# Kernel optimization log

Measured on AMD Instinct MI355X. Metric: run time of the kernel, lower is better.

## Reference

```python
import jax, jax.numpy as jnp
import numpy as np

NUM_HEADS = 8

def _feature_map(t):
    return jax.nn.elu(t) + 1.0

def setup_inputs() -> dict:
    key = jax.random.key(0)
    ks = jax.random.split(key, 7)
    B, S, D = 2, 1024, 512
    sc = 1.0 / np.sqrt(D)
    return {
        'x':  jax.random.normal(ks[0], (B, S, D), dtype=jnp.float32),
        'Wq': jax.random.normal(ks[1], (D, D), dtype=jnp.float32) * sc,
        'Wk': jax.random.normal(ks[2], (D, D), dtype=jnp.float32) * sc,
        'Wv': jax.random.normal(ks[3], (D, D), dtype=jnp.float32) * sc,
        'Wo': jax.random.normal(ks[4], (D, D), dtype=jnp.float32) * sc,
        'bo': jnp.zeros((D,), dtype=jnp.float32),
        'Wg': jax.random.normal(ks[5], (2 * D, D), dtype=jnp.float32) * (1.0 / np.sqrt(2 * D)),
        'bg': jnp.zeros((D,), dtype=jnp.float32),
    }

def reference(x, Wq, Wk, Wv, Wo, bo, Wg, bg):
    B, S, D = x.shape
    H = NUM_HEADS
    hd = D // H
    # projections, split heads -> [B,S,H,hd]
    q = _feature_map((x @ Wq).reshape(B, S, H, hd))
    k = _feature_map((x @ Wk).reshape(B, S, H, hd))
    v = (x @ Wv).reshape(B, S, H, hd)
    # causal linear attention via cumulative sums
    kv = jnp.einsum('bshd,bshe->bshde', k, v)        # [B,S,H,hd,hd]
    kv_cumsum = jnp.cumsum(kv, axis=1)
    k_cumsum = jnp.cumsum(k, axis=1)
    numerator = jnp.einsum('bshd,bshde->bshe', q, kv_cumsum)
    denominator = jnp.einsum('bshd,bshd->bsh', q, k_cumsum)[..., None]
    out = (numerator / (denominator + 1e-6)).reshape(B, S, D)
    out = out @ Wo + bo
    gate = jax.nn.sigmoid(jnp.concatenate([x, out], axis=-1) @ Wg + bg)
    return x + gate * (out - x)
```

## Files before the change

kernel.cpp:

```cpp
#include <hip/hip_runtime.h>
#include <hip/hip_bf16.h>
#include <math.h>


typedef __bf16 bf16x8 __attribute__((ext_vector_type(8)));
typedef __bf16 bf16x4 __attribute__((ext_vector_type(4)));
typedef float f32x4 __attribute__((ext_vector_type(4)));

#define MFMA16(a, b, c) __builtin_amdgcn_mfma_f32_16x16x32_bf16(a, b, c, 0, 0, 0)

__device__ __forceinline__ float elu1(float v) { return v > 0.f ? v + 1.f : __expf(v); }

__device__ __forceinline__ void gload16(const void* g, void* l) {
    __builtin_amdgcn_global_load_lds((const __attribute__((address_space(1))) void*)g,
                                     (__attribute__((address_space(3))) void*)l, 16, 0, 0);
}

__global__ __launch_bounds__(256) void prep_kernel(
    const float* __restrict__ x, const float* __restrict__ Wq, const float* __restrict__ Wk,
    const float* __restrict__ Wv, const float* __restrict__ Wo, const float* __restrict__ Wg,
    __bf16* __restrict__ xb, __bf16* __restrict__ wqkvT, __bf16* __restrict__ woT,
    __bf16* __restrict__ wgT) {
    int z = blockIdx.z;
    if (z == 5) {
        int bid = blockIdx.y * 16 + blockIdx.x;
        int base = (bid * 256 + threadIdx.x) * 8;
        bf16x8 o;
#pragma unroll
        for (int j = 0; j < 8; j++) o[j] = (__bf16)x[base + j];
        *(bf16x8*)&xb[base] = o;
        return;
    }
    const float* in;
    __bf16* out;
    int R = 512, C = 512;
    if (z == 0) { in = Wq; out = wqkvT; }
    else if (z == 1) { in = Wk; out = wqkvT + (size_t)512 * 512; }
    else if (z == 2) { in = Wv; out = wqkvT + (size_t)1024 * 512; }
    else if (z == 3) { in = Wo; out = woT; }
    else { in = Wg; out = wgT; R = 1024; }
    if ((int)blockIdx.y * 32 >= R) return;
    __shared__ float t[32][33];
    int bx = blockIdx.x, by = blockIdx.y;
    int tx = threadIdx.x & 31, ty = threadIdx.x >> 5;
#pragma unroll
    for (int i = 0; i < 32; i += 8)
        t[ty + i][tx] = in[(size_t)(by * 32 + ty + i) * C + bx * 32 + tx];
    __syncthreads();
#pragma unroll
    for (int i = 0; i < 32; i += 8)
        out[(size_t)(bx * 32 + ty + i) * R + by * 32 + tx] = (__bf16)t[tx][ty + i];
}

template <int MODE, int BM, int BN>
__global__ __launch_bounds__(256) void gemm_kernel(
    const __bf16* __restrict__ A, const __bf16* __restrict__ A2,
    const __bf16* __restrict__ Bw, const float* __restrict__ bias,
    const float* __restrict__ xf, const float* __restrict__ proj,
    float* __restrict__ outf, __bf16* __restrict__ outb,
    __bf16* __restrict__ q_out, __bf16* __restrict__ k_out,
    __bf16* __restrict__ kt_out, __bf16* __restrict__ vt_out, int K) {
    constexpr int MI = BM / 32, NI = BN / 32;
    constexpr int LA = BM / 64, LB = BN / 64;
    constexpr int L = LA + LB;
    __shared__ __bf16 sA[4 * BM * 32];
    __shared__ __bf16 sB[4 * BN * 32];
    __shared__ __bf16 sE[(MODE == 0) ? 64 * 72 : 1];
    int bm = blockIdx.x, bn = blockIdx.y;
    int tid = threadIdx.x, w = tid >> 6, l = tid & 63;
    int wr = (w >> 1) * (16 * MI), wc = (w & 1) * (16 * NI);
    int r = tid >> 2, c = (tid & 3) * 8;
    f32x4 acc[MI][NI] = {};
    const int nt = K / 32;

    auto stage = [&](int t, int buf) {
        int k0 = t * 32;
        const __bf16* a0 = A;
        int gka = k0, lda = K;
        if (MODE == 2) {
            lda = 512;
            if (k0 >= 512) { a0 = A2; gka = k0 - 512; }
        }
#pragma unroll
        for (int i = 0; i < LA; i++)
            gload16(&a0[(size_t)(bm * BM + i * 64 + r) * lda + gka + c],
                    &sA[buf * (BM * 32) + i * 2048 + w * 512]);
#pragma unroll
        for (int i = 0; i < LB; i++)
            gload16(&Bw[(size_t)(bn * BN + i * 64 + r) * K + k0 + c],
                    &sB[buf * (BN * 32) + i * 2048 + w * 512]);
    };

    stage(0, 0);
    stage(1, 1);
    stage(2, 2);
    for (int t = 0; t < nt; t++) {
        if (t + 2 < nt) {
            if constexpr (L == 2) asm volatile("s_waitcnt vmcnt(4)" ::: "memory");
            else asm volatile("s_waitcnt vmcnt(6)" ::: "memory");
        } else if (t + 1 < nt) {
            if constexpr (L == 2) asm volatile("s_waitcnt vmcnt(2)" ::: "memory");
            else asm volatile("s_waitcnt vmcnt(3)" ::: "memory");
        } else {
            asm volatile("s_waitcnt vmcnt(0)" ::: "memory");
        }
        asm volatile("s_barrier" ::: "memory");
        if (t + 3 < nt) stage(t + 3, (t + 3) & 3);
        int buf = t & 3;
        bf16x8 af[MI], bfr[NI];
#pragma unroll
        for (int mi = 0; mi < MI; mi++)
            af[mi] = *(const bf16x8*)&sA[buf * (BM * 32) + (wr + mi * 16 + (l & 15)) * 32 + ((l >> 4) << 3)];
#pragma unroll
        for (int ni = 0; ni < NI; ni++)
            bfr[ni] = *(const bf16x8*)&sB[buf * (BN * 32) + (wc + ni * 16 + (l & 15)) * 32 + ((l >> 4) << 3)];
#pragma unroll
        for (int mi = 0; mi < MI; mi++)
#pragma unroll
            for (int ni = 0; ni < NI; ni++)
                acc[mi][ni] = MFMA16(af[mi], bfr[ni], acc[mi][ni]);
    }

    if (MODE == 0) {
        __syncthreads();
#pragma unroll
        for (int mi = 0; mi < MI; mi++)
#pragma unroll
            for (int ni = 0; ni < NI; ni++)
#pragma unroll
                for (int j = 0; j < 4; j++) {
                    int lr = wr + mi * 16 + ((l >> 4) << 2) + j;
                    int lc = wc + ni * 16 + (l & 15);
                    float v = acc[mi][ni][j];
                    if (bn < 16) v = elu1(v);
                    sE[lr * 72 + lc] = (__bf16)v;
                }
        __syncthreads();
        int which = bn >> 3;
        int b = bm >> 4, s0b = (bm & 15) * 64, h = bn & 7;
        int bh = b * 8 + h;
        if (which == 0 || which == 1) {
            __bf16* qk = (which == 0 ? q_out : k_out) + ((size_t)(bh * 1024 + s0b)) * 64;
#pragma unroll
            for (int p = 0; p < 2; p++) {
                int idx = p * 256 + tid;
                *(bf16x8*)&qk[idx * 8] = *(const bf16x8*)&sE[(idx >> 3) * 72 + (idx & 7) * 8];
            }
        }
        if (which >= 1) {
            __bf16* tdst = (which == 1 ? kt_out : vt_out) + (size_t)(bh * 64) * 1024 + s0b;
            alignas(16) __bf16 tmp[16];
#pragma unroll
            for (int sj = 0; sj < 16; sj++) tmp[sj] = sE[(w * 16 + sj) * 72 + l];
            *(bf16x8*)&tdst[(size_t)l * 1024 + w * 16] = *(const bf16x8*)&tmp[0];
            *(bf16x8*)&tdst[(size_t)l * 1024 + w * 16 + 8] = *(const bf16x8*)&tmp[8];
        }
    } else {
#pragma unroll
        for (int mi = 0; mi < MI; mi++)
#pragma unroll
            for (int ni = 0; ni < NI; ni++)
#pragma unroll
                for (int j = 0; j < 4; j++) {
                    int gm = bm * BM + wr + mi * 16 + ((l >> 4) << 2) + j;
                    int gn = bn * BN + wc + ni * 16 + (l & 15);
                    float v = acc[mi][ni][j] + bias[gn];
                    if (MODE == 1) {
                        outf[(size_t)gm * 512 + gn] = v;
                        outb[(size_t)gm * 512 + gn] = (__bf16)v;
                    } else {
                        float g = 1.f / (1.f + __expf(-v));
                        float xv = xf[(size_t)gm * 512 + gn];
                        float pv = proj[(size_t)gm * 512 + gn];
                        outf[(size_t)gm * 512 + gn] = xv + g * (pv - xv);
                    }
                }
    }
}

__global__ __launch_bounds__(256) void mc_kernel(const __bf16* __restrict__ ktb,
                                                 const __bf16* __restrict__ vtb,
                                                 float* __restrict__ Mc, float* __restrict__ ksc) {
    int blk = blockIdx.x;
    int bh = blk >> 3, ch = blk & 7;
    int tid = threadIdx.x, w = tid >> 6, l = tid & 63;
    const __bf16* vb = vtb + (size_t)bh * 65536 + ch * 128;
    const __bf16* kp = ktb + (size_t)bh * 65536 + ch * 128;
    f32x4 macc[4] = {};
#pragma unroll
    for (int ks = 0; ks < 4; ks++) {
        bf16x8 a = *(const bf16x8*)&vb[(size_t)(w * 16 + (l & 15)) * 1024 + ks * 32 + ((l >> 4) << 3)];
#pragma unroll
        for (int ni = 0; ni < 4; ni++) {
            bf16x8 bb = *(const bf16x8*)&kp[(size_t)(ni * 16 + (l & 15)) * 1024 + ks * 32 + ((l >> 4) << 3)];
            macc[ni] = MFMA16(a, bb, macc[ni]);
        }
    }
    float* mout = Mc + (size_t)blk * 4096;
#pragma unroll
    for (int ni = 0; ni < 4; ni++)
#pragma unroll
        for (int j = 0; j < 4; j++)
            mout[(size_t)(w * 16 + ((l >> 4) << 2) + j) * 64 + ni * 16 + (l & 15)] = macc[ni][j];
    if (tid < 64) {
        float s = 0.f;
        const __bf16* kr = ktb + (size_t)(bh * 64 + tid) * 1024 + ch * 128;
#pragma unroll
        for (int t = 0; t < 16; t++) {
            bf16x8 v = *(const bf16x8*)&kr[t * 8];
#pragma unroll
            for (int j = 0; j < 8; j++) s += (float)v[j];
        }
        ksc[blk * 64 + tid] = s;
    }
}

__global__ __launch_bounds__(256) void attn_kernel(
    const __bf16* __restrict__ qb, const __bf16* __restrict__ kb,
    const __bf16* __restrict__ vtb, const float* __restrict__ Mc,
    const float* __restrict__ ksc, __bf16* __restrict__ attn_out) {
    int blk = blockIdx.x;
    int bh = blk >> 4, ch = (blk >> 1) & 7, half = blk & 1;
    int b = bh >> 3, h = bh & 7;
    int tid = threadIdx.x, w = tid >> 6, l = tid & 63;

    __shared__ __bf16 sQ[64 * 72];
    __shared__ __bf16 sP[64 * 136];
    __shared__ __bf16 sM[64 * 72];
    __shared__ float den[64];
    __shared__ float rsum[64];
    __shared__ float ksst[64];

    const __bf16* qsrc = qb + (size_t)(bh * 1024 + ch * 128 + half * 64) * 64;
#pragma unroll
    for (int i = 0; i < 2; i++) {
        int e = i * 2048 + tid * 8;
        *(bf16x8*)&sQ[(e >> 6) * 72 + (e & 63)] = *(const bf16x8*)&qsrc[e];
    }
    {
        int r0 = tid >> 2, c0 = (tid & 3) * 16;
        f32x4 s0 = {}, s1 = {}, s2 = {}, s3 = {};
        const float* mcb = Mc + (size_t)(bh * 8) * 4096 + r0 * 64 + c0;
        for (int c = 0; c < ch; c++) {
            const float* p = mcb + (size_t)c * 4096;
            s0 += *(const f32x4*)&p[0];
            s1 += *(const f32x4*)&p[4];
            s2 += *(const f32x4*)&p[8];
            s3 += *(const f32x4*)&p[12];
        }
        __bf16* d = &sM[r0 * 72 + c0];
#pragma unroll
        for (int j = 0; j < 4; j++) {
            d[j] = (__bf16)s0[j];
            d[4 + j] = (__bf16)s1[j];
            d[8 + j] = (__bf16)s2[j];
            d[12 + j] = (__bf16)s3[j];
        }
    }
    if (tid < 64) {
        float s = 0.f;
        for (int c = 0; c < ch; c++) s += ksc[(bh * 8 + c) * 64 + tid];
        ksst[tid] = s;
    }
    __syncthreads();

    if (tid < 64) {
        float s = 0.f;
#pragma unroll
        for (int d0 = 0; d0 < 64; d0 += 8) {
            bf16x8 qv = *(const bf16x8*)&sQ[tid * 72 + d0];
#pragma unroll
            for (int jj = 0; jj < 8; jj++) s += (float)qv[jj] * ksst[d0 + jj];
        }
        den[tid] = s;
    }

    {
        int wr = w * 16;
        const int CFMAX = half ? (w + 4) : w;
        const int CFLIM = half ? 7 : 3;
        const __bf16* kbase = kb + (size_t)(bh * 1024 + ch * 128) * 64;
        bf16x8 aq[2];
#pragma unroll
        for (int ks = 0; ks < 2; ks++)
            aq[ks] = *(const bf16x8*)&sQ[(wr + (l & 15)) * 72 + ks * 32 + ((l >> 4) << 3)];
        f32x4 acc[8] = {};
#pragma unroll
        for (int cf = 0; cf < 8; cf++) {
            if (cf <= CFMAX && cf <= CFLIM) {
#pragma unroll
                for (int ks = 0; ks < 2; ks++) {
                    bf16x8 bfr = *(const bf16x8*)&kbase[(size_t)(cf * 16 + (l & 15)) * 64 + ks * 32 + ((l >> 4) << 3)];
                    acc[cf] = MFMA16(aq[ks], bfr, acc[cf]);
                }
            }
        }
#pragma unroll
        for (int j = 0; j < 4; j++) {
            int lrow = wr + ((l >> 4) << 2) + j;
            int grow = half * 64 + lrow;
            float rs = 0.f;
#pragma unroll
            for (int cf = 0; cf < 8; cf++) {
                if (cf <= CFMAX && cf <= CFLIM) {
                    int col = cf * 16 + (l & 15);
                    float v = acc[cf][j];
                    v = (col <= grow) ? v : 0.f;
                    rs += v;
                    sP[lrow * 136 + col] = (__bf16)v;
                }
            }
            if (CFMAX + 1 <= CFLIM) sP[lrow * 136 + (CFMAX + 1) * 16 + (l & 15)] = (__bf16)0.f;
#pragma unroll
            for (int off = 1; off < 16; off <<= 1) rs += __shfl_xor(rs, off);
            if ((l & 15) == 0) rsum[lrow] = rs;
        }
    }
    __syncthreads();

    f32x4 o[4] = {};
    {
        int wr = w * 16;
        int ksmax = half ? (2 + (w >> 1)) : (w >> 1);
        const __bf16* vbase = vtb + (size_t)bh * 65536 + ch * 128;
#pragma unroll
        for (int ks = 0; ks < 4; ks++) {
            if (ks <= ksmax) {
                bf16x8 a = *(const bf16x8*)&sP[(wr + (l & 15)) * 136 + ks * 32 + ((l >> 4) << 3)];
#pragma unroll
                for (int ni = 0; ni < 4; ni++) {
                    bf16x8 bfr = *(const bf16x8*)&vbase[(size_t)(ni * 16 + (l & 15)) * 1024 + ks * 32 + ((l >> 4) << 3)];
                    o[ni] = MFMA16(a, bfr, o[ni]);
                }
            }
        }
        if (ch > 0) {
#pragma unroll
            for (int ks = 0; ks < 2; ks++) {
                bf16x8 a = *(const bf16x8*)&sQ[(wr + (l & 15)) * 72 + ks * 32 + ((l >> 4) << 3)];
#pragma unroll
                for (int ni = 0; ni < 4; ni++) {
                    bf16x8 bfr = *(const bf16x8*)&sM[(ni * 16 + (l & 15)) * 72 + ks * 32 + ((l >> 4) << 3)];
                    o[ni] = MFMA16(a, bfr, o[ni]);
                }
            }
        }
    }

    __bf16* obase = attn_out + ((size_t)(b * 1024 + ch * 128 + half * 64)) * 512 + h * 64;
#pragma unroll
    for (int j = 0; j < 4; j++) {
        int lrow = w * 16 + ((l >> 4) << 2) + j;
        float dn = den[lrow] + rsum[lrow] + 1e-6f;
#pragma unroll
        for (int ni = 0; ni < 4; ni++) {
            int col = ni * 16 + (l & 15);
            obase[(size_t)lrow * 512 + col] = (__bf16)(o[ni][j] / dn);
        }
    }
}

extern "C" void kernel_launch(void* const* d_in, const int* in_sizes, int n_in,
                              void* d_out, int out_size, void* d_ws, size_t ws_size,
                              hipStream_t stream) {
    const float* x = (const float*)d_in[0];
    const float* Wq = (const float*)d_in[1];
    const float* Wk = (const float*)d_in[2];
    const float* Wv = (const float*)d_in[3];
    const float* Wo = (const float*)d_in[4];
    const float* bo = (const float*)d_in[5];
    const float* Wg = (const float*)d_in[6];
    const float* bg = (const float*)d_in[7];
    float* out = (float*)d_out;

    char* ws = (char*)d_ws;
    size_t off = 0;
    auto alloc = [&](size_t bytes) -> void* {
        void* p = ws + off;
        off += (bytes + 255) & ~(size_t)255;
        return p;
    };
    __bf16* xb    = (__bf16*)alloc((size_t)2048 * 512 * 2);
    __bf16* wqkvT = (__bf16*)alloc((size_t)1536 * 512 * 2);
    __bf16* woT   = (__bf16*)alloc((size_t)512 * 512 * 2);
    __bf16* wgT   = (__bf16*)alloc((size_t)512 * 1024 * 2);
    __bf16* qb    = (__bf16*)alloc((size_t)16 * 1024 * 64 * 2);
    __bf16* kb    = (__bf16*)alloc((size_t)16 * 1024 * 64 * 2);
    __bf16* ktb   = (__bf16*)alloc((size_t)16 * 64 * 1024 * 2);
    __bf16* vtb   = (__bf16*)alloc((size_t)16 * 64 * 1024 * 2);
    float*  Mc    = (float*)alloc((size_t)128 * 4096 * 4);
    float*  ksc   = (float*)alloc((size_t)128 * 64 * 4);
    __bf16* attn  = (__bf16*)alloc((size_t)2048 * 512 * 2);
    float*  proj  = (float*)alloc((size_t)2048 * 512 * 4);
    __bf16* projb = (__bf16*)alloc((size_t)2048 * 512 * 2);

    prep_kernel<<<dim3(16, 32, 6), 256, 0, stream>>>(x, Wq, Wk, Wv, Wo, Wg, xb, wqkvT, woT, wgT);
    gemm_kernel<0, 64, 64><<<dim3(32, 24), 256, 0, stream>>>(
        xb, nullptr, wqkvT, nullptr, nullptr, nullptr, nullptr, nullptr, qb, kb, ktb, vtb, 512);
    mc_kernel<<<128, 256, 0, stream>>>(ktb, vtb, Mc, ksc);
    attn_kernel<<<256, 256, 0, stream>>>(qb, kb, vtb, Mc, ksc, attn);
    gemm_kernel<1, 64, 64><<<dim3(32, 8), 256, 0, stream>>>(
        attn, nullptr, woT, bo, nullptr, nullptr, proj, projb, nullptr, nullptr, nullptr, nullptr, 512);
    gemm_kernel<2, 64, 64><<<dim3(32, 8), 256, 0, stream>>>(
        xb, projb, wgT, bg, x, proj, out, nullptr, nullptr, nullptr, nullptr, nullptr, 1024);
}
```

Baseline: 64.33 us.

## Move x-half of gate GEMM into QKV GEMM and drop fp32 proj buffer

The gate weight is split into its x part and its out part. The x part is appended to the fused QKV weight, so the first GEMM also computes x@Wg_x (stored as bf16). The gate GEMM then has K=512 instead of 1024 and adds the precomputed partial sum. The fp32 projection output is removed and the bf16 copy is reused in the blend, which cuts writes and reads but adds bf16 rounding to the partial gate sum and the out value.

```diff
diff --git a/kernel.cpp b/kernel.cpp
--- a/kernel.cpp
+++ b/kernel.cpp
@@ -20,7 +20,7 @@
     const float* __restrict__ x, const float* __restrict__ Wq, const float* __restrict__ Wk,
     const float* __restrict__ Wv, const float* __restrict__ Wo, const float* __restrict__ Wg,
     __bf16* __restrict__ xb, __bf16* __restrict__ wqkvT, __bf16* __restrict__ woT,
-    __bf16* __restrict__ wgT) {
+    __bf16* __restrict__ wg2T) {
     int z = blockIdx.z;
     if (z == 5) {
         int bid = blockIdx.y * 16 + blockIdx.x;
@@ -32,34 +32,41 @@
         return;
     }
     const float* in;
-    __bf16* out;
-    int R = 512, C = 512;
-    if (z == 0) { in = Wq; out = wqkvT; }
-    else if (z == 1) { in = Wk; out = wqkvT + (size_t)512 * 512; }
-    else if (z == 2) { in = Wv; out = wqkvT + (size_t)1024 * 512; }
-    else if (z == 3) { in = Wo; out = woT; }
-    else { in = Wg; out = wgT; R = 1024; }
+    int R = 512;
+    if (z == 0) in = Wq;
+    else if (z == 1) in = Wk;
+    else if (z == 2) in = Wv;
+    else if (z == 3) in = Wo;
+    else { in = Wg; R = 1024; }
     if ((int)blockIdx.y * 32 >= R) return;
     __shared__ float t[32][33];
     int bx = blockIdx.x, by = blockIdx.y;
     int tx = threadIdx.x & 31, ty = threadIdx.x >> 5;
 #pragma unroll
     for (int i = 0; i < 32; i += 8)
-        t[ty + i][tx] = in[(size_t)(by * 32 + ty + i) * C + bx * 32 + tx];
+        t[ty + i][tx] = in[(size_t)(by * 32 + ty + i) * 512 + bx * 32 + tx];
     __syncthreads();
 #pragma unroll
-    for (int i = 0; i < 32; i += 8)
-        out[(size_t)(bx * 32 + ty + i) * R + by * 32 + tx] = (__bf16)t[tx][ty + i];
+    for (int i = 0; i < 32; i += 8) {
+        int n = bx * 32 + ty + i;
+        int kk = by * 32 + tx;
+        __bf16 val = (__bf16)t[tx][ty + i];
+        if (z == 0) wqkvT[(size_t)n * 512 + kk] = val;
+        else if (z == 1) wqkvT[(size_t)(512 + n) * 512 + kk] = val;
+        else if (z == 2) wqkvT[(size_t)(1024 + n) * 512 + kk] = val;
+        else if (z == 3) woT[(size_t)n * 512 + kk] = val;
+        else if (kk < 512) wqkvT[(size_t)(1536 + n) * 512 + kk] = val;
+        else wg2T[(size_t)n * 512 + (kk - 512)] = val;
+    }
 }
 
 template <int MODE, int BM, int BN>
 __global__ __launch_bounds__(256) void gemm_kernel(
-    const __bf16* __restrict__ A, const __bf16* __restrict__ A2,
-    const __bf16* __restrict__ Bw, const float* __restrict__ bias,
-    const float* __restrict__ xf, const float* __restrict__ proj,
+    const __bf16* __restrict__ A, const __bf16* __restrict__ Bw, const float* __restrict__ bias,
+    const float* __restrict__ xf, const __bf16* __restrict__ xgb, const __bf16* __restrict__ pvb,
     float* __restrict__ outf, __bf16* __restrict__ outb,
     __bf16* __restrict__ q_out, __bf16* __restrict__ k_out,
-    __bf16* __restrict__ kt_out, __bf16* __restrict__ vt_out, int K) {
+    __bf16* __restrict__ kt_out, __bf16* __restrict__ vt_out, __bf16* __restrict__ xg_out, int K) {
     constexpr int MI = BM / 32, NI = BN / 32;
     constexpr int LA = BM / 64, LB = BN / 64;
     constexpr int L = LA + LB;
@@ -75,15 +82,9 @@
 
     auto stage = [&](int t, int buf) {
         int k0 = t * 32;
-        const __bf16* a0 = A;
-        int gka = k0, lda = K;
-        if (MODE == 2) {
-            lda = 512;
-            if (k0 >= 512) { a0 = A2; gka = k0 - 512; }
-        }
 #pragma unroll
         for (int i = 0; i < LA; i++)
-            gload16(&a0[(size_t)(bm * BM + i * 64 + r) * lda + gka + c],
+            gload16(&A[(size_t)(bm * BM + i * 64 + r) * K + k0 + c],
                     &sA[buf * (BM * 32) + i * 2048 + w * 512]);
 #pragma unroll
         for (int i = 0; i < LB; i++)
@@ -147,7 +148,7 @@
                 *(bf16x8*)&qk[idx * 8] = *(const bf16x8*)&sE[(idx >> 3) * 72 + (idx & 7) * 8];
             }
         }
-        if (which >= 1) {
+        if (which == 1 || which == 2) {
             __bf16* tdst = (which == 1 ? kt_out : vt_out) + (size_t)(bh * 64) * 1024 + s0b;
             alignas(16) __bf16 tmp[16];
 #pragma unroll
@@ -155,6 +156,15 @@
             *(bf16x8*)&tdst[(size_t)l * 1024 + w * 16] = *(const bf16x8*)&tmp[0];
             *(bf16x8*)&tdst[(size_t)l * 1024 + w * 16 + 8] = *(const bf16x8*)&tmp[8];
         }
+        if (which == 3) {
+            __bf16* dst = xg_out + (size_t)(bm * 64) * 512 + (bn - 24) * 64;
+#pragma unroll
+            for (int p = 0; p < 2; p++) {
+                int idx = p * 256 + tid;
+                *(bf16x8*)&dst[(size_t)(idx >> 3) * 512 + (idx & 7) * 8] =
+                    *(const bf16x8*)&sE[(idx >> 3) * 72 + (idx & 7) * 8];
+            }
+        }
     } else {
 #pragma unroll
         for (int mi = 0; mi < MI; mi++)
@@ -164,14 +174,14 @@
                 for (int j = 0; j < 4; j++) {
                     int gm = bm * BM + wr + mi * 16 + ((l >> 4) << 2) + j;
                     int gn = bn * BN + wc + ni * 16 + (l & 15);
-                    float v = acc[mi][ni][j] + bias[gn];
                     if (MODE == 1) {
-                        outf[(size_t)gm * 512 + gn] = v;
+                        float v = acc[mi][ni][j] + bias[gn];
                         outb[(size_t)gm * 512 + gn] = (__bf16)v;
                     } else {
+                        float v = acc[mi][ni][j] + (float)xgb[(size_t)gm * 512 + gn] + bias[gn];
                         float g = 1.f / (1.f + __expf(-v));
                         float xv = xf[(size_t)gm * 512 + gn];
-                        float pv = proj[(size_t)gm * 512 + gn];
+                        float pv = (float)pvb[(size_t)gm * 512 + gn];
                         outf[(size_t)gm * 512 + gn] = xv + g * (pv - xv);
                     }
                 }
@@ -381,9 +391,9 @@
         return p;
     };
     __bf16* xb    = (__bf16*)alloc((size_t)2048 * 512 * 2);
-    __bf16* wqkvT = (__bf16*)alloc((size_t)1536 * 512 * 2);
+    __bf16* wqkvT = (__bf16*)alloc((size_t)2048 * 512 * 2);
     __bf16* woT   = (__bf16*)alloc((size_t)512 * 512 * 2);
-    __bf16* wgT   = (__bf16*)alloc((size_t)512 * 1024 * 2);
+    __bf16* wg2T  = (__bf16*)alloc((size_t)512 * 512 * 2);
     __bf16* qb    = (__bf16*)alloc((size_t)16 * 1024 * 64 * 2);
     __bf16* kb    = (__bf16*)alloc((size_t)16 * 1024 * 64 * 2);
     __bf16* ktb   = (__bf16*)alloc((size_t)16 * 64 * 1024 * 2);
@@ -391,16 +401,19 @@
     float*  Mc    = (float*)alloc((size_t)128 * 4096 * 4);
     float*  ksc   = (float*)alloc((size_t)128 * 64 * 4);
     __bf16* attn  = (__bf16*)alloc((size_t)2048 * 512 * 2);
-    float*  proj  = (float*)alloc((size_t)2048 * 512 * 4);
     __bf16* projb = (__bf16*)alloc((size_t)2048 * 512 * 2);
-
-    prep_kernel<<<dim3(16, 32, 6), 256, 0, stream>>>(x, Wq, Wk, Wv, Wo, Wg, xb, wqkvT, woT, wgT);
-    gemm_kernel<0, 64, 64><<<dim3(32, 24), 256, 0, stream>>>(
-        xb, nullptr, wqkvT, nullptr, nullptr, nullptr, nullptr, nullptr, qb, kb, ktb, vtb, 512);
+    __bf16* xgb   = (__bf16*)alloc((size_t)2048 * 512 * 2);
+
+    prep_kernel<<<dim3(16, 32, 6), 256, 0, stream>>>(x, Wq, Wk, Wv, Wo, Wg, xb, wqkvT, woT, wg2T);
+    gemm_kernel<0, 64, 64><<<dim3(32, 32), 256, 0, stream>>>(
+        xb, wqkvT, nullptr, nullptr, nullptr, nullptr, nullptr, nullptr,
+        qb, kb, ktb, vtb, xgb, 512);
     mc_kernel<<<128, 256, 0, stream>>>(ktb, vtb, Mc, ksc);
     attn_kernel<<<256, 256, 0, stream>>>(qb, kb, vtb, Mc, ksc, attn);
     gemm_kernel<1, 64, 64><<<dim3(32, 8), 256, 0, stream>>>(
-        attn, nullptr, woT, bo, nullptr, nullptr, proj, projb, nullptr, nullptr, nullptr, nullptr, 512);
+        attn, woT, bo, nullptr, nullptr, nullptr, nullptr, projb,
+        nullptr, nullptr, nullptr, nullptr, nullptr, 512);
     gemm_kernel<2, 64, 64><<<dim3(32, 8), 256, 0, stream>>>(
-        xb, projb, wgT, bg, x, proj, out, nullptr, nullptr, nullptr, nullptr, nullptr, 1024);
-}
+        projb, wg2T, bg, x, xgb, projb, out, nullptr,
+        nullptr, nullptr, nullptr, nullptr, nullptr, 512);
+}
```

Result: faster. 62.98 us (-2.1%).
